# Kernel optimization log

Measured on AMD Instinct MI355X. Metric: run time of the kernel, lower is better.

The kernel has to match this reference:

```python
import jax, jax.numpy as jnp
import numpy as np
import math

B, LQ, LK, D = 8, 2048, 2048, 1024  # hidden_dim = O_dim = D


def setup_inputs() -> dict:
    key = jax.random.key(0)
    ks = jax.random.split(key, 9)
    s = 1.0 / math.sqrt(D)
    return {
        "key": jax.random.normal(ks[0], (B, LK, D), dtype=jnp.float32),
        "query": jax.random.normal(ks[1], (B, LQ, D), dtype=jnp.float32),
        "mask": jax.random.randint(ks[2], (B, LK), 0, 2, dtype=jnp.int32),
        "Wq": jax.random.uniform(ks[3], (D, D), jnp.float32, -s, s),
        "bq": jax.random.uniform(ks[4], (D,), jnp.float32, -s, s),
        "Wk": jax.random.uniform(ks[5], (D, D), jnp.float32, -s, s),
        "bk": jax.random.uniform(ks[6], (D,), jnp.float32, -s, s),
        "Wv": jax.random.uniform(ks[7], (D, D), jnp.float32, -s, s),
        "bv": jax.random.uniform(ks[8], (D,), jnp.float32, -s, s),
    }


def reference(key, query, mask, Wq, bq, Wk, bk, Wv, bv):
    # Linear projections (torch nn.Linear: x @ W.T + b)
    q = jnp.einsum("bld,hd->blh", query, Wq) + bq          # [B, LQ, H]
    k = jnp.einsum("bld,hd->blh", key, Wk) + bk            # [B, LK, H]
    # Quirk of original module: values Linear is applied to the PROJECTED key
    v = jnp.einsum("blh,oh->blo", k, Wv) + bv              # [B, LK, O]
    score = jnp.einsum("bqh,bkh->bqk", q, k) / math.sqrt(D)
    # mask_score: mask [B, LK] -> [B, 1, LK], fill zeros with -1e9
    score = jnp.where(mask[:, None, :] == 0, jnp.float32(-1e9), score)
    score = jax.nn.softmax(score, axis=-1)
    # dropout in eval mode = identity; NaN cleanup preserved
    score = jnp.where(jnp.isnan(score), jnp.float32(0.0), score)
    output = jnp.einsum("bqk,bko->bqo", score, v)
    return output, score
```

## Files before the change

### kernel.cpp

```cpp
#include <hip/hip_runtime.h>
#include <cstdint>

#define DDIM 1024
#define LQN  2048
#define LKN  2048
#define BBAT 8


typedef short bf16x8 __attribute__((ext_vector_type(8)));
typedef float f32x4  __attribute__((ext_vector_type(4)));

__device__ __forceinline__ unsigned short f2bf(float f) {
    union { float f; unsigned int i; } x; x.f = f;
    unsigned int r = (x.i + 0x7fffu + ((x.i >> 16) & 1u)) >> 16;
    return (unsigned short)r;
}
__device__ __forceinline__ bf16x8 cvt8(const float* p) {
    float4 x0 = *(const float4*)p;
    float4 x1 = *(const float4*)(p + 4);
    bf16x8 r;
    r[0] = (short)f2bf(x0.x); r[1] = (short)f2bf(x0.y);
    r[2] = (short)f2bf(x0.z); r[3] = (short)f2bf(x0.w);
    r[4] = (short)f2bf(x1.x); r[5] = (short)f2bf(x1.y);
    r[6] = (short)f2bf(x1.z); r[7] = (short)f2bf(x1.w);
    return r;
}

__device__ __forceinline__ void gl2lds16(const void* g, void* l) {
    __builtin_amdgcn_global_load_lds(
        reinterpret_cast<const __attribute__((address_space(1))) void*>(
            reinterpret_cast<uintptr_t>(g)),
        reinterpret_cast<__attribute__((address_space(3))) void*>(
            (unsigned)reinterpret_cast<uintptr_t>(l)),
        16, 0, 0);
}

__global__ __launch_bounds__(256)
void cast_bf16(const float* __restrict__ in, unsigned short* __restrict__ out,
               long n8)
{
    long i = (long)blockIdx.x * blockDim.x + threadIdx.x;
    const long stride = (long)gridDim.x * blockDim.x;
    for (; i < n8; i += stride)
        *(bf16x8*)(out + i * 8) = cvt8(in + i * 8);
}

template<int MODE>
__global__ __launch_bounds__(512)
void gemm_nt(const unsigned short* __restrict__ A,
             const unsigned short* __restrict__ B,
             const float* __restrict__ bias,
             const int* __restrict__ mask,
             void* __restrict__ out)
{
    constexpr int K   = (MODE == 3) ? LKN : DDIM;
    constexpr int LDA = K;
    constexpr int LDB = K;
    constexpr int NT  = K / 32;

    __shared__ unsigned short lds[3 * 16384];

    const int t    = threadIdx.x;
    const int lane = t & 63;
    const int wave = t >> 6;
    const int wm   = wave >> 2;
    const int wn   = wave & 3;

    const int gx   = gridDim.x;
    const int nwg  = gx * gridDim.y;
    const int bid0 = blockIdx.y * gx + blockIdx.x;
    const int bid  = ((nwg & 7) == 0) ? ((bid0 & 7) * (nwg >> 3) + (bid0 >> 3))
                                      : bid0;
    const int bm = bid / gx;
    const int bn = bid % gx;
    const int z  = blockIdx.z;

    const unsigned short* Ap = A;
    const unsigned short* Bp = B;
    if (MODE == 2) { Ap += (long)z * LQN * DDIM; Bp += (long)z * LKN * DDIM; }
    if (MODE == 3) { Ap += (long)z * LQN * LKN;  Bp += (long)z * DDIM * LKN; }

    const int srow = t >> 2;
    const int skk  = ((t & 3) ^ ((t >> 3) & 3)) * 8;
    const unsigned short* ga0 = Ap + (long)(bm * 256 + srow) * LDA + skk;
    const unsigned short* ga1 = ga0 + 128L * LDA;
    const unsigned short* gb0 = Bp + (long)(bn * 256 + srow) * LDB + skk;
    const unsigned short* gb1 = gb0 + 128L * LDB;
    const int woff = wave * 512;

    f32x4 acc[8][4];
    #pragma unroll
    for (int i = 0; i < 8; ++i)
        #pragma unroll
        for (int j = 0; j < 4; ++j)
            acc[i][j] = (f32x4)(0.0f);

    const int quad = lane >> 4;
    const int l15  = lane & 15;
    const int qoff = (quad ^ ((l15 >> 1) & 3)) * 8;

#define STAGE(bi, kt) do {                                              \
        unsigned short* sb = &lds[(bi) * 16384];                        \
        const int ko = (kt) * 32;                                       \
        gl2lds16(ga0 + ko, sb + woff);                                  \
        gl2lds16(ga1 + ko, sb + 4096  + woff);                          \
        gl2lds16(gb0 + ko, sb + 8192  + woff);                          \
        gl2lds16(gb1 + ko, sb + 12288 + woff);                          \
    } while (0)

    STAGE(0, 0);
    STAGE(1, 1);
    asm volatile("s_waitcnt vmcnt(4)" ::: "memory");
    __builtin_amdgcn_s_barrier();

    int cb = 0;
    for (int tt = 0; tt < NT; ++tt) {
        const int nb = (cb + 2 >= 3) ? (cb - 1) : (cb + 2);
        const bool st = (tt + 2 < NT);
        if (st) STAGE(nb, tt + 2);

        const unsigned short* sb = &lds[cb * 16384];
        bf16x8 af[8], bfv[4];
        #pragma unroll
        for (int j = 0; j < 4; ++j)
            bfv[j] = *(const bf16x8*)&sb[8192 + (wn * 64 + j * 16 + l15) * 32 + qoff];
        #pragma unroll
        for (int i = 0; i < 8; ++i)
            af[i] = *(const bf16x8*)&sb[(wm * 128 + i * 16 + l15) * 32 + qoff];

        __builtin_amdgcn_s_setprio(1);
        #pragma unroll
        for (int i = 0; i < 8; ++i)
            #pragma unroll
            for (int j = 0; j < 4; ++j)
                acc[i][j] = __builtin_amdgcn_mfma_f32_16x16x32_bf16(
                    af[i], bfv[j], acc[i][j], 0, 0, 0);
        __builtin_amdgcn_s_setprio(0);

        if (st) asm volatile("s_waitcnt vmcnt(4)" ::: "memory");
        else    asm volatile("s_waitcnt vmcnt(0)" ::: "memory");
        __builtin_amdgcn_s_barrier();
        cb = (cb + 1 >= 3) ? 0 : (cb + 1);
    }
#undef STAGE

    #pragma unroll
    for (int i = 0; i < 8; ++i) {
        #pragma unroll
        for (int j = 0; j < 4; ++j) {
            const int grow = bm * 256 + wm * 128 + i * 16 + quad * 4;
            const int gcol = bn * 256 + wn * 64 + j * 16 + l15;
            if (MODE == 0) {
                const float bc = bias[gcol];
                #pragma unroll
                for (int r = 0; r < 4; ++r)
                    ((unsigned short*)out)[(long)(grow + r) * DDIM + gcol] =
                        f2bf(acc[i][j][r] + bc);
            } else if (MODE == 1) {
                const int b2 = gcol >> 11;
                const int lk = gcol & 2047;
                #pragma unroll
                for (int r = 0; r < 4; ++r) {
                    const float bc = bias[grow + r];
                    ((unsigned short*)out)[(long)b2 * DDIM * LKN +
                                           (long)(grow + r) * LKN + lk] =
                        f2bf(acc[i][j][r] + bc);
                }
            } else if (MODE == 2) {
                const int mv = mask[z * LKN + gcol];
                #pragma unroll
                for (int r = 0; r < 4; ++r) {
                    float v = acc[i][j][r] * 0.03125f;
                    if (mv == 0) v = -1e9f;
                    ((float*)out)[(long)z * LQN * LKN +
                                  (long)(grow + r) * LKN + gcol] = v;
                }
            } else {
                #pragma unroll
                for (int r = 0; r < 4; ++r)
                    ((float*)out)[(long)z * LQN * DDIM +
                                  (long)(grow + r) * DDIM + gcol] = acc[i][j][r];
            }
        }
    }
}

__global__ __launch_bounds__(256)
void softmax_rows(float* __restrict__ P, unsigned short* __restrict__ Pb)
{
    const int t = threadIdx.x;
    const long base = (long)blockIdx.x * LKN + t * 8;

    float4 r0 = *(const float4*)&P[base];
    float4 r1 = *(const float4*)&P[base + 4];
    float v[8] = { r0.x, r0.y, r0.z, r0.w, r1.x, r1.y, r1.z, r1.w };

    float m = -3.0e38f;
    #pragma unroll
    for (int i = 0; i < 8; ++i) m = fmaxf(m, v[i]);
    #pragma unroll
    for (int off = 32; off >= 1; off >>= 1) m = fmaxf(m, __shfl_xor(m, off, 64));
    __shared__ float redm[4];
    if ((t & 63) == 0) redm[t >> 6] = m;
    __syncthreads();
    m = fmaxf(fmaxf(redm[0], redm[1]), fmaxf(redm[2], redm[3]));

    float s = 0.0f;
    #pragma unroll
    for (int i = 0; i < 8; ++i) { v[i] = __expf(v[i] - m); s += v[i]; }
    #pragma unroll
    for (int off = 32; off >= 1; off >>= 1) s += __shfl_xor(s, off, 64);
    __shared__ float reds[4];
    if ((t & 63) == 0) reds[t >> 6] = s;
    __syncthreads();
    s = reds[0] + reds[1] + reds[2] + reds[3];

    const float inv = 1.0f / s;
    r0.x = v[0] * inv; r0.y = v[1] * inv; r0.z = v[2] * inv; r0.w = v[3] * inv;
    r1.x = v[4] * inv; r1.y = v[5] * inv; r1.z = v[6] * inv; r1.w = v[7] * inv;
    *(float4*)&P[base]     = r0;
    *(float4*)&P[base + 4] = r1;

    bf16x8 pb;
    pb[0] = (short)f2bf(r0.x); pb[1] = (short)f2bf(r0.y);
    pb[2] = (short)f2bf(r0.z); pb[3] = (short)f2bf(r0.w);
    pb[4] = (short)f2bf(r1.x); pb[5] = (short)f2bf(r1.y);
    pb[6] = (short)f2bf(r1.z); pb[7] = (short)f2bf(r1.w);
    *(bf16x8*)&Pb[base] = pb;
}

extern "C" void kernel_launch(void* const* d_in, const int* in_sizes, int n_in,
                              void* d_out, int out_size, void* d_ws, size_t ws_size,
                              hipStream_t stream)
{
    (void)in_sizes; (void)n_in; (void)out_size;

    const float* key   = (const float*)d_in[0];
    const float* query = (const float*)d_in[1];
    const int*   mask  = (const int*)d_in[2];
    const float* Wq    = (const float*)d_in[3];
    const float* bq    = (const float*)d_in[4];
    const float* Wk    = (const float*)d_in[5];
    const float* bk    = (const float*)d_in[6];
    const float* Wv    = (const float*)d_in[7];
    const float* bv    = (const float*)d_in[8];

    float* outO = (float*)d_out;
    float* outP = outO + (size_t)BBAT * LQN * DDIM;

    unsigned short* Wqb  = (unsigned short*)d_ws;
    unsigned short* Wkb  = Wqb + (size_t)DDIM * DDIM;
    unsigned short* Wvb  = Wkb + (size_t)DDIM * DDIM;
    unsigned short* gbuf = Wvb + (size_t)DDIM * DDIM;

    const size_t fixed = (size_t)3 * DDIM * DDIM * sizeof(unsigned short);
    const size_t perB  = ((size_t)LQN * LKN + (size_t)3 * LQN * DDIM) *
                         sizeof(unsigned short);
    size_t avail = (ws_size > fixed) ? (ws_size - fixed) : 0;
    int g = (int)(avail / perB);
    if (g > BBAT) g = BBAT;
    if (g < 1)    g = 1;

    dim3 blk(256, 1, 1);
    dim3 gblk(512, 1, 1);

    cast_bf16<<<dim3(512, 1, 1), blk, 0, stream>>>(Wq, Wqb, (long)DDIM * DDIM / 8);
    cast_bf16<<<dim3(512, 1, 1), blk, 0, stream>>>(Wk, Wkb, (long)DDIM * DDIM / 8);
    cast_bf16<<<dim3(512, 1, 1), blk, 0, stream>>>(Wv, Wvb, (long)DDIM * DDIM / 8);

    for (int b0 = 0; b0 < BBAT; b0 += g) {
        const int gl = (BBAT - b0 < g) ? (BBAT - b0) : g;

        unsigned short* regionA = gbuf;
        unsigned short* qc = regionA;
        unsigned short* kc = regionA + (size_t)gl * LQN * DDIM;
        unsigned short* Pb = regionA;
        unsigned short* Qp = regionA + (size_t)gl * LQN * LKN;
        unsigned short* Kp = Qp + (size_t)gl * LQN * DDIM;
        unsigned short* Vt = Kp + (size_t)gl * LKN * DDIM;

        cast_bf16<<<dim3(2048, 1, 1), blk, 0, stream>>>(
            query + (size_t)b0 * LQN * DDIM, qc, (long)gl * LQN * DDIM / 8);
        cast_bf16<<<dim3(2048, 1, 1), blk, 0, stream>>>(
            key + (size_t)b0 * LKN * DDIM, kc, (long)gl * LKN * DDIM / 8);

        gemm_nt<0><<<dim3(4, gl * 8, 1), gblk, 0, stream>>>(qc, Wqb, bq, nullptr, Qp);

        gemm_nt<0><<<dim3(4, gl * 8, 1), gblk, 0, stream>>>(kc, Wkb, bk, nullptr, Kp);

        gemm_nt<1><<<dim3(gl * 8, 4, 1), gblk, 0, stream>>>(Wvb, Kp, bv, nullptr, Vt);

        gemm_nt<2><<<dim3(8, 8, gl), gblk, 0, stream>>>(
            Qp, Kp, nullptr, mask + (size_t)b0 * LKN,
            outP + (size_t)b0 * LQN * LKN);

        softmax_rows<<<dim3(gl * LQN, 1, 1), blk, 0, stream>>>(
            outP + (size_t)b0 * LQN * LKN, Pb);

        gemm_nt<3><<<dim3(4, 8, gl), gblk, 0, stream>>>(
            Pb, Vt, nullptr, nullptr, outO + (size_t)b0 * LQN * DDIM);
    }
}
```

Before: 612.0 us.

## Deepen GEMM pipeline to four LDS stages and interleave loads with MFMA halves

Raises the LDS ring from three to four buffers so prefetch runs three K-tiles ahead. Each iteration is split into two MFMA halves, and the A and B global-to-LDS loads for the next stage are issued between them, with extra barriers. The tile remap now folds the batch dimension into the grouped block ordering. The aim is to hide global memory latency and spread issue pressure. In exchange it uses more shared memory, which may lower occupancy, and adds barriers.

```diff
diff --git a/kernel.cpp b/kernel.cpp
--- a/kernel.cpp
+++ b/kernel.cpp
@@ -58,7 +58,7 @@
     constexpr int LDB = K;
     constexpr int NT  = K / 32;
 
-    __shared__ unsigned short lds[3 * 16384];
+    __shared__ unsigned short lds[4 * 16384];
 
     const int t    = threadIdx.x;
     const int lane = t & 63;
@@ -66,14 +66,16 @@
     const int wm   = wave >> 2;
     const int wn   = wave & 3;
 
-    const int gx   = gridDim.x;
-    const int nwg  = gx * gridDim.y;
-    const int bid0 = blockIdx.y * gx + blockIdx.x;
-    const int bid  = ((nwg & 7) == 0) ? ((bid0 & 7) * (nwg >> 3) + (bid0 >> 3))
-                                      : bid0;
-    const int bm = bid / gx;
-    const int bn = bid % gx;
-    const int z  = blockIdx.z;
+    const int gx  = gridDim.x;
+    const int gy  = gridDim.y;
+    const int nwg = gx * gy * gridDim.z;
+    int lin = (blockIdx.z * gy + blockIdx.y) * gx + blockIdx.x;
+    if ((nwg & 7) == 0) lin = (lin & 7) * (nwg >> 3) + (lin >> 3);
+    const int plane = gx * gy;
+    const int z   = lin / plane;
+    const int rem = lin - z * plane;
+    const int bm  = rem / gx;
+    const int bn  = rem - (rem / gx) * gx;
 
     const unsigned short* Ap = A;
     const unsigned short* Bp = B;
@@ -100,47 +102,71 @@
     const int qoff = (quad ^ ((l15 >> 1) & 3)) * 8;
 
 #define STAGE(bi, kt) do {                                              \
-        unsigned short* sb = &lds[(bi) * 16384];                        \
+        unsigned short* sbw = &lds[(bi) * 16384];                       \
         const int ko = (kt) * 32;                                       \
-        gl2lds16(ga0 + ko, sb + woff);                                  \
-        gl2lds16(ga1 + ko, sb + 4096  + woff);                          \
-        gl2lds16(gb0 + ko, sb + 8192  + woff);                          \
-        gl2lds16(gb1 + ko, sb + 12288 + woff);                          \
+        gl2lds16(ga0 + ko, sbw + woff);                                 \
+        gl2lds16(ga1 + ko, sbw + 4096  + woff);                         \
+        gl2lds16(gb0 + ko, sbw + 8192  + woff);                         \
+        gl2lds16(gb1 + ko, sbw + 12288 + woff);                         \
     } while (0)
 
     STAGE(0, 0);
     STAGE(1, 1);
-    asm volatile("s_waitcnt vmcnt(4)" ::: "memory");
+    STAGE(2, 2);
+    asm volatile("s_waitcnt vmcnt(8)" ::: "memory");
     __builtin_amdgcn_s_barrier();
 
-    int cb = 0;
     for (int tt = 0; tt < NT; ++tt) {
-        const int nb = (cb + 2 >= 3) ? (cb - 1) : (cb + 2);
-        const bool st = (tt + 2 < NT);
-        if (st) STAGE(nb, tt + 2);
-
-        const unsigned short* sb = &lds[cb * 16384];
-        bf16x8 af[8], bfv[4];
+        const unsigned short* sb = &lds[(tt & 3) * 16384];
+        unsigned short* nbuf = &lds[((tt + 3) & 3) * 16384];
+        const int  ko = (tt + 3) * 32;
+        const bool st = (tt + 3 < NT);
+
+        bf16x8 bfv[4], af[4];
         #pragma unroll
         for (int j = 0; j < 4; ++j)
             bfv[j] = *(const bf16x8*)&sb[8192 + (wn * 64 + j * 16 + l15) * 32 + qoff];
         #pragma unroll
-        for (int i = 0; i < 8; ++i)
+        for (int i = 0; i < 4; ++i)
             af[i] = *(const bf16x8*)&sb[(wm * 128 + i * 16 + l15) * 32 + qoff];
-
+        if (st) {
+            gl2lds16(ga0 + ko, nbuf + woff);
+            gl2lds16(ga1 + ko, nbuf + 4096 + woff);
+        }
+        __builtin_amdgcn_s_barrier();
+        asm volatile("s_waitcnt lgkmcnt(0)" ::: "memory");
         __builtin_amdgcn_s_setprio(1);
         #pragma unroll
-        for (int i = 0; i < 8; ++i)
+        for (int i = 0; i < 4; ++i)
             #pragma unroll
             for (int j = 0; j < 4; ++j)
                 acc[i][j] = __builtin_amdgcn_mfma_f32_16x16x32_bf16(
                     af[i], bfv[j], acc[i][j], 0, 0, 0);
         __builtin_amdgcn_s_setprio(0);
 
-        if (st) asm volatile("s_waitcnt vmcnt(4)" ::: "memory");
-        else    asm volatile("s_waitcnt vmcnt(0)" ::: "memory");
+        bf16x8 af2[4];
+        #pragma unroll
+        for (int i = 0; i < 4; ++i)
+            af2[i] = *(const bf16x8*)&sb[(wm * 128 + 64 + i * 16 + l15) * 32 + qoff];
+        if (st) {
+            gl2lds16(gb0 + ko, nbuf + 8192 + woff);
+            gl2lds16(gb1 + ko, nbuf + 12288 + woff);
+        }
         __builtin_amdgcn_s_barrier();
-        cb = (cb + 1 >= 3) ? 0 : (cb + 1);
+        asm volatile("s_waitcnt lgkmcnt(0)" ::: "memory");
+        __builtin_amdgcn_s_setprio(1);
+        #pragma unroll
+        for (int i = 0; i < 4; ++i)
+            #pragma unroll
+            for (int j = 0; j < 4; ++j)
+                acc[i + 4][j] = __builtin_amdgcn_mfma_f32_16x16x32_bf16(
+                    af2[i], bfv[j], acc[i + 4][j], 0, 0, 0);
+        __builtin_amdgcn_s_setprio(0);
+
+        if (tt < NT - 3)       asm volatile("s_waitcnt vmcnt(8)" ::: "memory");
+        else if (tt == NT - 3) asm volatile("s_waitcnt vmcnt(4)" ::: "memory");
+        else                   asm volatile("s_waitcnt vmcnt(0)" ::: "memory");
+        __builtin_amdgcn_s_barrier();
     }
 #undef STAGE
 
```

Result: no change. 607.3 us (-0.8%).
